# Performance work log

Hardware: AMD Instinct MI355X
Metric: run time of the kernel (lower is better)

Reference implementation:

```python
import jax, jax.numpy as jnp
import numpy as np

B, C, H, W = 16, 512, 16, 64
T = 128
V, E, EH, DH = 600, 80, 256, 512


def _lstm_scan(x_seq, h0, c0, Wih, Whh, b):
    # x_seq: [S, N, in]; PyTorch gate order i,f,g,o
    def step(carry, x):
        h, c = carry
        g = x @ Wih.T + h @ Whh.T + b
        i, f, gg, o = jnp.split(g, 4, axis=-1)
        c_new = jax.nn.sigmoid(f) * c + jax.nn.sigmoid(i) * jnp.tanh(gg)
        h_new = jax.nn.sigmoid(o) * jnp.tanh(c_new)
        return (h_new, c_new), h_new
    (hT, cT), hs = jax.lax.scan(step, (h0, c0), x_seq)
    return hs, hT, cT


def setup_inputs():
    key = jax.random.key(0)
    ks = jax.random.split(key, 32)
    INIT = 0.01
    def u(k, shape, s):
        return jax.random.uniform(k, shape, jnp.float32, -s, s)
    se = 1.0 / np.sqrt(EH)
    sd = 1.0 / np.sqrt(DH)
    sc = 1.0 / np.sqrt(DH + 2 * EH)
    so = 1.0 / np.sqrt(EH)
    sv = 1.0 / np.sqrt(2 * EH)
    return {
        'features': jax.random.normal(ks[0], (B, C, H, W), jnp.float32),
        'formulas': jax.random.randint(ks[1], (B, T), 0, V),
        'Wih_f': u(ks[2], (4 * EH, C), se), 'Whh_f': u(ks[3], (4 * EH, EH), se),
        'bih_f': u(ks[4], (4 * EH,), se), 'bhh_f': u(ks[5], (4 * EH,), se),
        'Wih_b': u(ks[6], (4 * EH, C), se), 'Whh_b': u(ks[7], (4 * EH, EH), se),
        'bih_b': u(ks[8], (4 * EH,), se), 'bhh_b': u(ks[9], (4 * EH,), se),
        'emb': jax.random.normal(ks[10], (V, E), jnp.float32),
        'Wc_w': u(ks[11], (EH, DH + 2 * EH), sc), 'Wc_b': u(ks[12], (EH,), sc),
        'Wout_w': u(ks[13], (V, EH), so), 'Wout_b': u(ks[14], (V,), so),
        'Vh0': u(ks[15], (2, EH), INIT), 'Vc0': u(ks[16], (2, EH), INIT),
        'beta': u(ks[17], (DH,), INIT),
        'Wh_w': u(ks[18], (DH, DH), sd), 'Wh_b': u(ks[19], (DH,), sd),
        'Wv_w': u(ks[20], (DH, 2 * EH), sv), 'Wv_b': u(ks[21], (DH,), sv),
        'Wdec_ih': u(ks[22], (4 * DH, EH + E), sd), 'Wdec_hh': u(ks[23], (4 * DH, DH), sd),
        'bdec_ih': u(ks[24], (4 * DH,), sd), 'bdec_hh': u(ks[25], (4 * DH,), sd),
    }


def _forward(features, formulas, Wih_f, Whh_f, bih_f, bhh_f, Wih_b, Whh_b, bih_b, bhh_b,
             emb, Wc_w, Wc_b, Wout_w, Wout_b, Vh0, Vc0, beta, Wh_w, Wh_b, Wv_w, Wv_b,
             Wdec_ih, Wdec_hh, bdec_ih, bdec_hh):
    Bv, Cv, Hv, Wd = features.shape
    eh = Vh0.shape[1]
    # ---- row encoder: bidirectional LSTM over width, batch = B*H ----
    x = features.transpose(0, 2, 3, 1).reshape(Bv * Hv, Wd, Cv).transpose(1, 0, 2)  # [W, B*H, C]
    h0f = jnp.broadcast_to(Vh0[0], (Bv * Hv, eh)); c0f = jnp.broadcast_to(Vc0[0], (Bv * Hv, eh))
    h0b = jnp.broadcast_to(Vh0[1], (Bv * Hv, eh)); c0b = jnp.broadcast_to(Vc0[1], (Bv * Hv, eh))
    hs_f, hTf, cTf = _lstm_scan(x, h0f, c0f, Wih_f, Whh_f, bih_f + bhh_f)
    hs_b, hTb, cTb = _lstm_scan(x[::-1], h0b, c0b, Wih_b, Whh_b, bih_b + bhh_b)
    hs_b = hs_b[::-1]
    enc_out = jnp.concatenate([hs_f, hs_b], -1).transpose(1, 0, 2).reshape(Bv, Hv, Wd, 2 * eh)

    def convert(s):  # [2, B*H, eh] -> [B, 2*eh]: permute, merge directions, mean over H
        return s.reshape(2, Bv, Hv, eh).transpose(1, 2, 0, 3).reshape(Bv, Hv, 2 * eh).mean(axis=1)
    h0 = convert(jnp.stack([hTf, hTb]))
    c0 = convert(jnp.stack([cTf, cTb]))
    ctx0 = enc_out.mean(axis=(1, 2))
    O0 = jnp.tanh(jnp.concatenate([h0, ctx0], 1) @ Wc_w.T + Wc_b)

    Wv_enc = enc_out @ Wv_w.T + Wv_b  # hoisted: W_v(enc_out) is constant across decode steps

    def dec_step(carry, tgt):
        h, c, O = carry
        prev_y = emb[tgt]                                   # [B, E]
        inp = jnp.concatenate([prev_y, O], 1)
        g = inp @ Wdec_ih.T + h @ Wdec_hh.T + bdec_ih + bdec_hh
        i, f, gg, o = jnp.split(g, 4, axis=-1)
        c_t = jax.nn.sigmoid(f) * c + jax.nn.sigmoid(i) * jnp.tanh(gg)
        h_t = jax.nn.sigmoid(o) * jnp.tanh(c_t)
        lin_h = h @ Wh_w.T + Wh_b                           # NB: attention uses PREVIOUS h, as in source
        e = jnp.sum(beta * jnp.tanh(lin_h[:, None, None, :] + Wv_enc), -1)  # [B, H, W]
        alpha = jax.nn.softmax(e.reshape(Bv, -1), -1).reshape(Bv, Hv, Wd)
        context = jnp.einsum('bhw,bhwd->bd', alpha, enc_out)
        O_t = jnp.tanh(jnp.concatenate([h_t, context], 1) @ Wc_w.T + Wc_b)
        logit = jax.nn.softmax(O_t @ Wout_w.T + Wout_b, -1)  # eval-mode softmax
        return (h_t, c_t, O_t), logit

    _, logits = jax.lax.scan(dec_step, (h0, c0, O0), formulas.T)
    return logits.transpose(1, 0, 2)  # [B, T, V]


def reference(features, formulas, Wih_f, Whh_f, bih_f, bhh_f, Wih_b, Whh_b, bih_b, bhh_b,
              emb, Wc_w, Wc_b, Wout_w, Wout_b, Vh0, Vc0, beta, Wh_w, Wh_b, Wv_w, Wv_b,
              Wdec_ih, Wdec_hh, bdec_ih, bdec_hh):
    logits = _forward(features, formulas, Wih_f, Whh_f, bih_f, bhh_f, Wih_b, Whh_b, bih_b, bhh_b,
                      emb, Wc_w, Wc_b, Wout_w, Wout_b, Vh0, Vc0, beta, Wh_w, Wh_b, Wv_w, Wv_b,
                      Wdec_ih, Wdec_hh, bdec_ih, bdec_hh)
    targets = jnp.argmax(logits, axis=2)  # argmax(log(p)) == argmax(p)
    return logits, targets
```

## Files before the change

### kernel.cpp

```cpp
#include <hip/hip_runtime.h>
#include <math.h>

#define NB 16
#define NC 512
#define NH 16
#define NW 64
#define NT 128
#define NV 600
#define NE 80
#define EH 256
#define DH 512
#define NSEQ 256
#define GEH 1024
#define GDH 2048

#define OFF_XPRE_F 0ull
#define OFF_XPRE_B 16777216ull
#define OFF_XT     33554432ull
#define OFF_ENC    41943040ull
#define OFF_WENC   50331648ull
#define OFF_WDT    50855936ull
#define OFF_WHT    52592640ull
#define OFF_WCT    52854784ull
#define OFF_WOUTT  53116928ull
#define OFF_HA     53270528ull
#define OFF_CENC   53532672ull
#define OFF_CDEC   53663744ull
#define OFF_CTX0   53671936ull
#define OFF_OKT    53680128ull
#define WS_FLOATS  53708800ull

__device__ __forceinline__ float sigf(float x) {
  return __builtin_amdgcn_rcpf(1.f + __expf(-x));
}
__device__ __forceinline__ float tanhfast(float x) {
  float e = __expf(2.f * x);
  return 1.f - 2.f * __builtin_amdgcn_rcpf(e + 1.f);
}

__global__ void k_transpose(float* __restrict__ dst, const float* __restrict__ src,
                            int R, int Cc) {
  int idx = blockIdx.x * 256 + threadIdx.x;
  if (idx >= R * Cc) return;
  int c = idx / R, r = idx - c * R;
  dst[idx] = src[(size_t)r * Cc + c];
}

__global__ void k_prep_wenc(float* __restrict__ dst, const float* __restrict__ whh, int dir) {
  int idx = blockIdx.x * 256 + threadIdx.x;
  int g = idx & 3, j = (idx >> 2) & 255, k = idx >> 10;
  dst[(size_t)dir * 262144 + idx] = whh[((size_t)(g * 256 + j)) * 256 + k];
}

__global__ void k_buildXt(float* __restrict__ Xt, const float* __restrict__ feat) {
  __shared__ float tile[64][65];
  int n = blockIdx.x, cb = blockIdx.y * 64;
  int b = n >> 4, hh = n & 15;
  int tid = threadIdx.x;
  for (int i = 0; i < 16; ++i) {
    int c = (tid >> 6) + i * 4;
    int w = tid & 63;
    tile[c][w] = feat[(((size_t)b * NC + cb + c) * NH + hh) * NW + w];
  }
  __syncthreads();
  for (int i = 0; i < 16; ++i) {
    int w = (tid >> 6) + i * 4;
    int ci = tid & 63;
    Xt[((size_t)(w * NSEQ + n)) * NC + cb + ci] = tile[ci][w];
  }
}

__global__ __launch_bounds__(256) void k_gemm_nt(
    const float* __restrict__ A, const float* __restrict__ Wt,
    const float* __restrict__ bias1, const float* __restrict__ bias2,
    float* __restrict__ Cout, int M, int Nn, int K) {
  __shared__ float As[128 * 32];
  __shared__ float Bs[128 * 32];
  int tid = threadIdx.x;
  int mb = blockIdx.x * 128, nb = blockIdx.y * 128;
  int tx = tid & 15, ty = tid >> 4;
  int row0 = ty * 8, col0 = tx * 8;
  float acc[8][8];
#pragma unroll
  for (int i = 0; i < 8; ++i)
#pragma unroll
    for (int j = 0; j < 8; ++j) acc[i][j] = 0.f;
  int lm = tid >> 1, lk = (tid & 1) * 8;
  int sw = 4 * ((lm >> 3) & 7);
  int p0 = (lk + sw) & 31, p1 = (lk + 4 + sw) & 31;
  const float* Ap = A + (size_t)(mb + lm) * K + lk;
  const float* Bp = Wt + (size_t)(nb + lm) * K + lk;
  for (int k0 = 0; k0 < K; k0 += 16) {
    float4 a0 = *(const float4*)(Ap + k0);
    float4 a1 = *(const float4*)(Ap + k0 + 4);
    float4 b0 = *(const float4*)(Bp + k0);
    float4 b1 = *(const float4*)(Bp + k0 + 4);
    __syncthreads();
    *(float4*)&As[lm * 32 + p0] = a0;
    *(float4*)&As[lm * 32 + p1] = a1;
    *(float4*)&Bs[lm * 32 + p0] = b0;
    *(float4*)&Bs[lm * 32 + p1] = b1;
    __syncthreads();
#pragma unroll
    for (int kq = 0; kq < 4; ++kq) {
      float4 av[8], bv[8];
#pragma unroll
      for (int i = 0; i < 8; ++i) {
        int m = row0 + i;
        av[i] = *(float4*)&As[m * 32 + ((kq * 4 + 4 * ((m >> 3) & 7)) & 31)];
      }
#pragma unroll
      for (int j = 0; j < 8; ++j) {
        int n = col0 + j;
        bv[j] = *(float4*)&Bs[n * 32 + ((kq * 4 + 4 * ((n >> 3) & 7)) & 31)];
      }
#pragma unroll
      for (int i = 0; i < 8; ++i)
#pragma unroll
        for (int j = 0; j < 8; ++j)
          acc[i][j] += av[i].x * bv[j].x + av[i].y * bv[j].y
                     + av[i].z * bv[j].z + av[i].w * bv[j].w;
    }
  }
  float bs[8];
#pragma unroll
  for (int j = 0; j < 8; ++j) {
    float v = bias1 ? bias1[nb + col0 + j] : 0.f;
    if (bias2) v += bias2[nb + col0 + j];
    bs[j] = v;
  }
  for (int i = 0; i < 8; ++i) {
    float* cp = Cout + (size_t)(mb + row0 + i) * Nn + nb + col0;
#pragma unroll
    for (int j = 0; j < 8; ++j) cp[j] = acc[i][j] + bs[j];
  }
}

__global__ __launch_bounds__(256) void k_encoder_s(
    const float* __restrict__ wenc, const float* __restrict__ xpreF,
    const float* __restrict__ xpreB, const float* __restrict__ Vh0,
    const float* __restrict__ Vc0, float* __restrict__ encout,
    float* __restrict__ hT_out, float* __restrict__ cT_out) {
  __shared__ float hs[4][256];
  int bid = blockIdx.x;
  int dir = bid >> 6;
  int s0 = (bid & 63) * 4;
  int j = threadIdx.x;
  float c[4];
  {
    float h0 = Vh0[dir * 256 + j];
    float c0v = Vc0[dir * 256 + j];
#pragma unroll
    for (int s = 0; s < 4; ++s) { hs[s][j] = h0; c[s] = c0v; }
  }
  __syncthreads();
  const float* wp = wenc + (size_t)dir * 262144 + (size_t)j * 4;
  const float* xbase = dir ? xpreB : xpreF;
  for (int t = 0; t < 64; ++t) {
    int w = dir ? (63 - t) : t;
    float acc[4][4];
#pragma unroll
    for (int s = 0; s < 4; ++s)
#pragma unroll
      for (int g = 0; g < 4; ++g) acc[s][g] = 0.f;
#pragma unroll 4
    for (int k = 0; k < 256; ++k) {
      float4 w4 = *(const float4*)(wp + (size_t)k * 1024);
      float h0k = hs[0][k], h1k = hs[1][k], h2k = hs[2][k], h3k = hs[3][k];
      acc[0][0] += w4.x * h0k; acc[0][1] += w4.y * h0k; acc[0][2] += w4.z * h0k; acc[0][3] += w4.w * h0k;
      acc[1][0] += w4.x * h1k; acc[1][1] += w4.y * h1k; acc[1][2] += w4.z * h1k; acc[1][3] += w4.w * h1k;
      acc[2][0] += w4.x * h2k; acc[2][1] += w4.y * h2k; acc[2][2] += w4.z * h2k; acc[2][3] += w4.w * h2k;
      acc[3][0] += w4.x * h3k; acc[3][1] += w4.y * h3k; acc[3][2] += w4.z * h3k; acc[3][3] += w4.w * h3k;
    }
    __syncthreads();
#pragma unroll
    for (int s = 0; s < 4; ++s) {
      int n = s0 + s;
      const float* xp = xbase + ((size_t)w * NSEQ + n) * GEH;
      float gi_ = acc[s][0] + xp[j];
      float gf_ = acc[s][1] + xp[j + 256];
      float gg_ = acc[s][2] + xp[j + 512];
      float go_ = acc[s][3] + xp[j + 768];
      float cn = sigf(gf_) * c[s] + sigf(gi_) * tanhfast(gg_);
      c[s] = cn;
      float hn = sigf(go_) * tanhfast(cn);
      hs[s][j] = hn;
      encout[((size_t)n * NW + w) * (2 * EH) + dir * EH + j] = hn;
    }
    __syncthreads();
  }
#pragma unroll
  for (int s = 0; s < 4; ++s) {
    int n = s0 + s;
    hT_out[((size_t)(dir * NSEQ + n)) * EH + j] = hs[s][j];
    cT_out[((size_t)(dir * NSEQ + n)) * EH + j] = c[s];
  }
}

__global__ void k_conv(const float* __restrict__ hA, const float* __restrict__ cE,
                       const float* __restrict__ enc, float* __restrict__ cdec,
                       float* __restrict__ okT, float* __restrict__ ctx0) {
  int b = blockIdx.x, tid = threadIdx.x;
  for (int d = tid; d < 512; d += 256) {
    float s = 0.f;
    for (int p = 0; p < 1024; ++p) s += enc[((size_t)b * 1024 + p) * 512 + d];
    ctx0[(size_t)b * 512 + d] = s * (1.f / 1024.f);
    int dir = d >> 8, u = d & 255;
    float sh = 0.f, sc_ = 0.f;
    for (int hh = 0; hh < 16; ++hh) {
      size_t idx = ((size_t)(dir * NSEQ + b * 16 + hh)) * EH + u;
      sh += hA[idx]; sc_ += cE[idx];
    }
    cdec[(size_t)b * 512 + d] = sc_ * (1.f / 16.f);
    okT[(size_t)(256 + d) * 16 + b] = sh * (1.f / 16.f);
  }
}

__global__ void k_O0v2(const float* __restrict__ okT, const float* __restrict__ ctx0,
                       const float* __restrict__ wcT, const float* __restrict__ wcb,
                       const float* __restrict__ whT, const float* __restrict__ whb,
                       float* __restrict__ okT_o, float* __restrict__ linh) {
  int b = blockIdx.x, tid = threadIdx.x;
  float a = wcb[tid];
  for (int k = 0; k < 512; ++k)
    a += okT[(size_t)(256 + k) * 16 + b] * wcT[(size_t)k * 256 + tid];
  const float* cb = ctx0 + (size_t)b * 512;
  for (int k = 0; k < 512; ++k)
    a += cb[k] * wcT[(size_t)(512 + k) * 256 + tid];
  okT_o[(size_t)tid * 16 + b] = tanhfast(a);
  for (int d = tid; d < 512; d += 256) {
    float v = whb[d];
    for (int k = 0; k < 512; ++k)
      v += okT[(size_t)(256 + k) * 16 + b] * whT[(size_t)k * 512 + d];
    linh[(size_t)b * 512 + d] = v;
  }
}

__global__ void k_embproj(const int* __restrict__ formulas, const float* __restrict__ emb,
                          const float* __restrict__ wdT, const float* __restrict__ b1,
                          const float* __restrict__ b2, float* __restrict__ ep) {
  int g = blockIdx.x * 256 + threadIdx.x;
  int tb = blockIdx.y;
  int b = tb & 15, t = tb >> 4;
  int tok = formulas[b * NT + t];
  const float* ev = emb + (size_t)tok * NE;
  float a = b1[g] + b2[g];
  for (int k = 0; k < NE; ++k) a += ev[k] * wdT[(size_t)k * GDH + g];
  ep[(size_t)tb * GDH + g] = a;
}

__device__ __forceinline__ void logits_block(
    int vc, int lane, int wq, const float* __restrict__ okT,
    const float* __restrict__ woutT, const float* __restrict__ woutb,
    float* __restrict__ ev, float* __restrict__ evp) {
  int v = vc * 64 + lane;
  bool valid = v < NV;
  int vl = valid ? v : (NV - 1);
  float acc[4] = {0.f, 0.f, 0.f, 0.f};
  for (int k = 0; k < 256; ++k) {
    float w = woutT[(size_t)k * NV + vl];
    float4 o4 = *(const float4*)&okT[(size_t)k * 16 + wq * 4];
    acc[0] += w * o4.x; acc[1] += w * o4.y; acc[2] += w * o4.z; acc[3] += w * o4.w;
  }
  float bs = woutb[vl];
#pragma unroll
  for (int i = 0; i < 4; ++i) {
    float e = valid ? __expf(acc[i] + bs) : 0.f;
    if (valid) ev[(size_t)(wq * 4 + i) * NV + v] = e;
    float s = e;
#pragma unroll
    for (int m = 1; m < 64; m <<= 1) s += __shfl_xor(s, m, 64);
    if (lane == 0) evp[(wq * 4 + i) * 16 + vc] = s;
  }
}

__device__ __forceinline__ void norm_block(
    int b, int tid, const float* __restrict__ ev, const float* __restrict__ evp,
    float* __restrict__ outp, int t) {
  float tot = 0.f;
#pragma unroll
  for (int i = 0; i < 10; ++i) tot += evp[b * 16 + i];
  float r = __builtin_amdgcn_rcpf(tot);
  float* orow = outp + ((size_t)b * NT + t) * NV;
  orow[tid] = ev[b * NV + tid] * r;
  orow[tid + 256] = ev[b * NV + tid + 256] * r;
  if (tid < 88) orow[tid + 512] = ev[b * NV + tid + 512] * r;
}

__global__ __launch_bounds__(256) void k_dec1(
    const float* __restrict__ okT, const float* __restrict__ wdT,
    const float* __restrict__ woutT, const float* __restrict__ woutb,
    const float* __restrict__ linh, const float* __restrict__ beta,
    const float* __restrict__ wvenc, const float* __restrict__ enc,
    float* __restrict__ gpart, float* __restrict__ ctxp,
    float* __restrict__ spart, float* __restrict__ ev, float* __restrict__ evp,
    int t) {
  __shared__ float smem[32];
  int bid = blockIdx.x, tid = threadIdx.x;
  int lane = tid & 63, wq = tid >> 6;

  if (bid < 512) {
    int b = bid >> 5, pc2 = bid & 31;
    int d0 = lane * 8;
    float lh[8], bt[8];
    const float* lp = linh + (size_t)b * 512 + d0;
#pragma unroll
    for (int jj = 0; jj < 8; ++jj) { lh[jj] = lp[jj]; bt[jj] = beta[d0 + jj]; }
#pragma unroll
    for (int pi = 0; pi < 8; ++pi) {
      int p = pc2 * 32 + wq * 8 + pi;
      const float* wvp = wvenc + ((size_t)(b * 1024 + p)) * 512 + d0;
      float e = 0.f;
#pragma unroll
      for (int jj = 0; jj < 8; ++jj) e += bt[jj] * tanhfast(lh[jj] + wvp[jj]);
#pragma unroll
      for (int m = 1; m < 64; m <<= 1) e += __shfl_xor(e, m, 64);
      if (lane == 0) smem[wq * 8 + pi] = __expf(e);
    }
    __syncthreads();
    float a0 = 0.f, a1 = 0.f;
    const float* erb = enc + ((size_t)(b * 1024 + pc2 * 32)) * 512 + tid * 2;
#pragma unroll 4
    for (int p = 0; p < 32; ++p) {
      float s = smem[p];
      float2 e2 = *(const float2*)(erb + (size_t)p * 512);
      a0 += s * e2.x;
      a1 += s * e2.y;
    }
    *(float2*)&ctxp[((size_t)(b * 32 + pc2)) * 512 + tid * 2] = make_float2(a0, a1);
    if (tid == 0) {
      float s = 0.f;
#pragma unroll
      for (int p = 0; p < 32; ++p) s += smem[p];
      spart[b * 32 + pc2] = s;
    }
  } else if (bid < 560) {
    int idx = bid - 512;
    int oc = idx / 6, kc = idx - oc * 6;
    int o = oc * 256 + tid, k0 = kc * 128;
    const float* wp = wdT + (size_t)(80 + k0) * GDH + o;
    const float* sp = okT + (size_t)k0 * 16;
    float acc[16];
#pragma unroll
    for (int i = 0; i < 16; ++i) acc[i] = 0.f;
    for (int kk = 0; kk < 128; ++kk) {
      float w = wp[(size_t)kk * GDH];
#pragma unroll
      for (int bb = 0; bb < 16; ++bb) acc[bb] += sp[kk * 16 + bb] * w;
    }
#pragma unroll
    for (int bb = 0; bb < 16; ++bb)
      gpart[((size_t)(kc * 16 + bb)) * GDH + o] = acc[bb];
  } else {
    if (t > 0) logits_block(bid - 560, lane, wq, okT, woutT, woutb, ev, evp);
  }
}

__global__ __launch_bounds__(256) void k_dec2(
    const float* __restrict__ gpart, const float* __restrict__ ep,
    const float* __restrict__ ctxp, const float* __restrict__ spart,
    const float* __restrict__ wcT, const float* __restrict__ wcb,
    const float* __restrict__ whT, const float* __restrict__ whb,
    const float* __restrict__ ev, const float* __restrict__ evp,
    float* __restrict__ cdecA, float* __restrict__ cdecB,
    float* __restrict__ okT, float* __restrict__ linh,
    float* __restrict__ outp, int t) {
  __shared__ float smem[1280];
  int bid = blockIdx.x, tid = threadIdx.x;
  if (bid < 64) {
    int b = bid >> 2, q = bid & 3;
    const float* cold = (t & 1) ? cdecB : cdecA;
    float* cnew = (t & 1) ? cdecA : cdecB;
    float Ssum = 0.f;
#pragma unroll
    for (int pc = 0; pc < 32; ++pc) Ssum += spart[b * 32 + pc];
    float rS = __builtin_amdgcn_rcpf(Ssum);
    {
      int d = tid * 2;
      float s0 = 0.f, s1 = 0.f;
#pragma unroll 4
      for (int pc = 0; pc < 32; ++pc) {
        float2 c2 = *(const float2*)&ctxp[((size_t)(b * 32 + pc)) * 512 + d];
        s0 += c2.x; s1 += c2.y;
      }
      smem[512 + d] = s0 * rS;
      smem[512 + d + 1] = s1 * rS;
    }
#pragma unroll
    for (int half = 0; half < 2; ++half) {
      int j = half * 256 + tid;
      float g4[4];
#pragma unroll
      for (int gi = 0; gi < 4; ++gi) {
        float v = ep[((size_t)(t * 16 + b)) * GDH + gi * 512 + j];
#pragma unroll
        for (int kc = 0; kc < 6; ++kc)
          v += gpart[((size_t)(kc * 16 + b)) * GDH + gi * 512 + j];
        g4[gi] = v;
      }
      size_t ci = (size_t)b * 512 + j;
      float cn = sigf(g4[1]) * cold[ci] + sigf(g4[0]) * tanhfast(g4[2]);
      cnew[ci] = cn;
      float hn = sigf(g4[3]) * tanhfast(cn);
      smem[j] = hn;
      okT[(size_t)(256 + j) * 16 + b] = hn;
    }
    __syncthreads();
    {
      int ol = tid & 63, kq = tid >> 6;
      int o = q * 64 + ol;
      float a = 0.f;
      const float* wp = wcT + (size_t)(kq * 256) * 256 + o;
      const float* sp = smem + kq * 256;
      for (int k = 0; k < 256; ++k) a += wp[(size_t)k * 256] * sp[k];
      smem[1024 + kq * 64 + ol] = a;
    }
    __syncthreads();
    if (tid < 64) {
      float s = smem[1024 + tid] + smem[1088 + tid] + smem[1152 + tid] + smem[1216 + tid];
      int o = q * 64 + tid;
      okT[(size_t)o * 16 + b] = tanhfast(s + wcb[o]);
    }
    __syncthreads();
    {
      int o2 = tid & 127, kh = tid >> 7;
      int o = q * 128 + o2;
      float a = 0.f;
      const float* wp = whT + (size_t)(kh * 256) * 512 + o;
      const float* sp = smem + kh * 256;
      for (int k = 0; k < 256; ++k) a += wp[(size_t)k * 512] * sp[k];
      smem[1024 + kh * 128 + o2] = a;
    }
    __syncthreads();
    if (tid < 128) {
      int o = q * 128 + tid;
      float s = smem[1024 + tid] + smem[1152 + tid];
      linh[(size_t)b * 512 + o] = s + whb[o];
    }
  } else {
    if (t > 0) norm_block(bid - 64, tid, ev, evp, outp, t - 1);
  }
}

__global__ __launch_bounds__(256) void k_log_tail(
    const float* __restrict__ okT, const float* __restrict__ woutT,
    const float* __restrict__ woutb, float* __restrict__ ev, float* __restrict__ evp) {
  int lane = threadIdx.x & 63, wq = threadIdx.x >> 6;
  logits_block(blockIdx.x, lane, wq, okT, woutT, woutb, ev, evp);
}

__global__ void k_norm(const float* __restrict__ ev, const float* __restrict__ evp,
                       float* __restrict__ outp, int t) {
  norm_block(blockIdx.x, threadIdx.x, ev, evp, outp, t);
}

__global__ void k_argmax(const float* __restrict__ outp, float* __restrict__ tgt) {
  int bt = blockIdx.x;
  int lane = threadIdx.x;
  const float* row = outp + (size_t)bt * NV;
  float bv = -1.f;
  int bi = 0;
  for (int v = lane; v < NV; v += 64) {
    float x = row[v];
    if (x > bv) { bv = x; bi = v; }
  }
#pragma unroll
  for (int m = 1; m < 64; m <<= 1) {
    float ov = __shfl_xor(bv, m, 64);
    int oi = __shfl_xor(bi, m, 64);
    if (ov > bv || (ov == bv && oi < bi)) { bv = ov; bi = oi; }
  }
  if (lane == 0) tgt[bt] = (float)bi;
}

extern "C" void kernel_launch(void* const* d_in, const int* in_sizes, int n_in,
                              void* d_out, int out_size, void* d_ws, size_t ws_size,
                              hipStream_t stream) {
  (void)in_sizes; (void)n_in; (void)out_size;
  if (ws_size < WS_FLOATS * sizeof(float)) return;

  const float* feat     = (const float*)d_in[0];
  const int*   formulas = (const int*)d_in[1];
  const float* Wih_f    = (const float*)d_in[2];
  const float* Whh_f    = (const float*)d_in[3];
  const float* bih_f    = (const float*)d_in[4];
  const float* bhh_f    = (const float*)d_in[5];
  const float* Wih_b    = (const float*)d_in[6];
  const float* Whh_b    = (const float*)d_in[7];
  const float* bih_b    = (const float*)d_in[8];
  const float* bhh_b    = (const float*)d_in[9];
  const float* emb      = (const float*)d_in[10];
  const float* Wc_w     = (const float*)d_in[11];
  const float* Wc_b     = (const float*)d_in[12];
  const float* Wout_w   = (const float*)d_in[13];
  const float* Wout_b   = (const float*)d_in[14];
  const float* Vh0      = (const float*)d_in[15];
  const float* Vc0      = (const float*)d_in[16];
  const float* beta     = (const float*)d_in[17];
  const float* Wh_w     = (const float*)d_in[18];
  const float* Wh_b     = (const float*)d_in[19];
  const float* Wv_w     = (const float*)d_in[20];
  const float* Wv_b     = (const float*)d_in[21];
  const float* Wdec_ih  = (const float*)d_in[22];
  const float* Wdec_hh  = (const float*)d_in[23];
  const float* bdec_ih  = (const float*)d_in[24];
  const float* bdec_hh  = (const float*)d_in[25];

  float* ws = (float*)d_ws;
  float* xpreF  = ws + OFF_XPRE_F;
  float* xpreB  = ws + OFF_XPRE_B;
  float* xt     = ws + OFF_XT;
  float* encout = ws + OFF_ENC;
  float* wenc   = ws + OFF_WENC;
  float* wdT    = ws + OFF_WDT;
  float* whT    = ws + OFF_WHT;
  float* wcT    = ws + OFF_WCT;
  float* woutT  = ws + OFF_WOUTT;
  float* hA     = ws + OFF_HA;
  float* cenc   = ws + OFF_CENC;
  float* cdecA  = ws + OFF_CDEC;
  float* ctx0   = ws + OFF_CTX0;
  float* okT    = ws + OFF_OKT;
  float* gpart  = xpreB;
  float* ctxp   = gpart + 196608;
  float* spart  = ctxp + 262144;
  float* ev     = spart + 512;
  float* evp    = ev + 9600;
  float* linh   = evp + 256;
  float* cdecB  = linh + 8192;
  float* embproj = xpreF;
  float* wvenc   = xt;

  float* out_logits = (float*)d_out;
  float* out_tgt    = out_logits + (size_t)NB * NT * NV;

  k_transpose<<<(2048 * 336 + 255) / 256, 256, 0, stream>>>(wdT, Wdec_ih, 2048, 336);
  k_transpose<<<(2048 * 512 + 255) / 256, 256, 0, stream>>>(wdT + 336 * 2048, Wdec_hh, 2048, 512);
  k_transpose<<<(512 * 512 + 255) / 256, 256, 0, stream>>>(whT, Wh_w, 512, 512);
  k_transpose<<<(256 * 1024 + 255) / 256, 256, 0, stream>>>(wcT, Wc_w, 256, 1024);
  k_transpose<<<(600 * 256 + 255) / 256, 256, 0, stream>>>(woutT, Wout_w, 600, 256);
  k_prep_wenc<<<1024, 256, 0, stream>>>(wenc, Whh_f, 0);
  k_prep_wenc<<<1024, 256, 0, stream>>>(wenc, Whh_b, 1);
  k_buildXt<<<dim3(256, 8), 256, 0, stream>>>(xt, feat);
  k_gemm_nt<<<dim3(128, 8), 256, 0, stream>>>(xt, Wih_f, bih_f, bhh_f, xpreF, 16384, 1024, 512);
  k_gemm_nt<<<dim3(128, 8), 256, 0, stream>>>(xt, Wih_b, bih_b, bhh_b, xpreB, 16384, 1024, 512);

  k_encoder_s<<<128, 256, 0, stream>>>(wenc, xpreF, xpreB, Vh0, Vc0, encout, hA, cenc);

  k_gemm_nt<<<dim3(128, 4), 256, 0, stream>>>(encout, Wv_w, Wv_b, nullptr, wvenc, 16384, 512, 512);
  k_conv<<<16, 256, 0, stream>>>(hA, cenc, encout, cdecA, okT, ctx0);
  k_O0v2<<<16, 256, 0, stream>>>(okT, ctx0, wcT, Wc_b, whT, Wh_b, okT, linh);
  k_embproj<<<dim3(8, 2048), 256, 0, stream>>>(formulas, emb, wdT, bdec_ih, bdec_hh, embproj);

  for (int t = 0; t < NT; ++t) {
    k_dec1<<<570, 256, 0, stream>>>(okT, wdT, woutT, Wout_b, linh, beta, wvenc, encout,
                                    gpart, ctxp, spart, ev, evp, t);
    k_dec2<<<80, 256, 0, stream>>>(gpart, embproj, ctxp, spart, wcT, Wc_b, whT, Wh_b,
                                   ev, evp, cdecA, cdecB, okT, linh, out_logits, t);
  }
  k_log_tail<<<10, 256, 0, stream>>>(okT, woutT, Wout_b, ev, evp);
  k_norm<<<16, 256, 0, stream>>>(ev, evp, out_logits, NT - 1);
  k_argmax<<<NB * NT, 64, 0, stream>>>(out_logits, out_tgt);
}
```

Measured before the change: 8.165 ms.

## Fuse decoder step kernels into one launch with intra-kernel flag synchronization

```diff
diff --git a/kernel.cpp b/kernel.cpp
--- a/kernel.cpp
+++ b/kernel.cpp
@@ -36,6 +36,18 @@
 __device__ __forceinline__ float tanhfast(float x) {
   float e = __expf(2.f * x);
   return 1.f - 2.f * __builtin_amdgcn_rcpf(e + 1.f);
+}
+
+__device__ __forceinline__ float ldc(const float* p) {
+  return __hip_atomic_load(p, __ATOMIC_RELAXED, __HIP_MEMORY_SCOPE_AGENT);
+}
+__device__ __forceinline__ void stc(float* p, float v) {
+  __hip_atomic_store(p, v, __ATOMIC_RELAXED, __HIP_MEMORY_SCOPE_AGENT);
+}
+__device__ __forceinline__ float2 ldc2(const float* p) {
+  unsigned long long u = __hip_atomic_load((const unsigned long long*)p,
+                                           __ATOMIC_RELAXED, __HIP_MEMORY_SCOPE_AGENT);
+  union { unsigned long long u; float2 f; } c; c.u = u; return c.f;
 }
 
 __global__ void k_transpose(float* __restrict__ dst, const float* __restrict__ src,
@@ -249,6 +261,37 @@
   ep[(size_t)tb * GDH + g] = a;
 }
 
+__global__ void k_zero(int* __restrict__ p, int n) {
+  int idx = blockIdx.x * 256 + threadIdx.x;
+  for (int i = idx; i < n; i += gridDim.x * 256) p[i] = 0;
+}
+
+__device__ __forceinline__ void logits_block_coh(
+    int vc, int lane, int wq, const float* __restrict__ okT,
+    const float* __restrict__ woutT, const float* __restrict__ woutb,
+    float* __restrict__ ev, float* __restrict__ evp) {
+  int v = vc * 64 + lane;
+  bool valid = v < NV;
+  int vl = valid ? v : (NV - 1);
+  float acc[4] = {0.f, 0.f, 0.f, 0.f};
+  for (int k = 0; k < 256; ++k) {
+    float w = woutT[(size_t)k * NV + vl];
+    float2 o01 = ldc2(&okT[(size_t)k * 16 + wq * 4]);
+    float2 o23 = ldc2(&okT[(size_t)k * 16 + wq * 4 + 2]);
+    acc[0] += w * o01.x; acc[1] += w * o01.y; acc[2] += w * o23.x; acc[3] += w * o23.y;
+  }
+  float bs = woutb[vl];
+#pragma unroll
+  for (int i = 0; i < 4; ++i) {
+    float e = valid ? __expf(acc[i] + bs) : 0.f;
+    if (valid) ev[(size_t)(wq * 4 + i) * NV + v] = e;
+    float s = e;
+#pragma unroll
+    for (int m = 1; m < 64; m <<= 1) s += __shfl_xor(s, m, 64);
+    if (lane == 0) evp[(wq * 4 + i) * 16 + vc] = s;
+  }
+}
+
 __device__ __forceinline__ void logits_block(
     int vc, int lane, int wq, const float* __restrict__ okT,
     const float* __restrict__ woutT, const float* __restrict__ woutb,
@@ -287,25 +330,165 @@
   if (tid < 88) orow[tid + 512] = ev[b * NV + tid + 512] * r;
 }
 
-__global__ __launch_bounds__(256) void k_dec1(
-    const float* __restrict__ okT, const float* __restrict__ wdT,
-    const float* __restrict__ woutT, const float* __restrict__ woutb,
-    const float* __restrict__ linh, const float* __restrict__ beta,
+__global__ __launch_bounds__(256, 3) void k_step(
+    float* __restrict__ okT, float* __restrict__ linh,
+    float* __restrict__ cdecA, float* __restrict__ cdecB,
+    const float* __restrict__ wdT, const float* __restrict__ whT,
+    const float* __restrict__ wcT, const float* __restrict__ woutT,
+    const float* __restrict__ whb, const float* __restrict__ beta,
+    const float* __restrict__ wcb, const float* __restrict__ woutb,
     const float* __restrict__ wvenc, const float* __restrict__ enc,
-    float* __restrict__ gpart, float* __restrict__ ctxp,
-    float* __restrict__ spart, float* __restrict__ ev, float* __restrict__ evp,
-    int t) {
-  __shared__ float smem[32];
+    const float* __restrict__ ep,
+    const float* __restrict__ gpart_r, const float* __restrict__ ctxp_r,
+    const float* __restrict__ spart_r,
+    float* __restrict__ gpart_w, float* __restrict__ ctxp_w,
+    float* __restrict__ spart_w,
+    float* __restrict__ ev_w, float* __restrict__ evp_w,
+    const float* __restrict__ ev_r, const float* __restrict__ evp_r,
+    float* __restrict__ outp, int* __restrict__ flg, int t) {
+  __shared__ float smem[1280];
   int bid = blockIdx.x, tid = threadIdx.x;
   int lane = tid & 63, wq = tid >> 6;
 
-  if (bid < 512) {
-    int b = bid >> 5, pc2 = bid & 31;
+  if (bid < 64) {
+    if (t == 0) return;
+    int tt = t - 1;
+    int b = bid >> 2, q = bid & 3;
+    const float* cold = (tt & 1) ? cdecB : cdecA;
+    float* cnew = (tt & 1) ? cdecA : cdecB;
+    float Ssum = 0.f;
+#pragma unroll
+    for (int pc = 0; pc < 32; ++pc) Ssum += spart_r[b * 32 + pc];
+    float rS = __builtin_amdgcn_rcpf(Ssum);
+    {
+      int d = tid * 2;
+      float s0 = 0.f, s1 = 0.f;
+#pragma unroll 4
+      for (int pc = 0; pc < 32; ++pc) {
+        float2 c2 = *(const float2*)&ctxp_r[((size_t)(b * 32 + pc)) * 512 + d];
+        s0 += c2.x; s1 += c2.y;
+      }
+      smem[512 + d] = s0 * rS;
+      smem[512 + d + 1] = s1 * rS;
+    }
+#pragma unroll
+    for (int half = 0; half < 2; ++half) {
+      int j = half * 256 + tid;
+      float g4[4];
+#pragma unroll
+      for (int gi = 0; gi < 4; ++gi) {
+        float v = ep[((size_t)(tt * 16 + b)) * GDH + gi * 512 + j];
+#pragma unroll
+        for (int kc = 0; kc < 6; ++kc)
+          v += gpart_r[((size_t)(kc * 16 + b)) * GDH + gi * 512 + j];
+        g4[gi] = v;
+      }
+      size_t ci = (size_t)b * 512 + j;
+      float cn = sigf(g4[1]) * cold[ci] + sigf(g4[0]) * tanhfast(g4[2]);
+      cnew[ci] = cn;
+      float hn = sigf(g4[3]) * tanhfast(cn);
+      smem[j] = hn;
+      stc(&okT[(size_t)(256 + j) * 16 + b], hn);
+    }
+    __syncthreads();
+    {
+      int ol = tid & 63, kq = tid >> 6;
+      int o = q * 64 + ol;
+      float a = 0.f;
+      const float* wp = wcT + (size_t)(kq * 256) * 256 + o;
+      const float* sp = smem + kq * 256;
+      for (int k = 0; k < 256; ++k) a += wp[(size_t)k * 256] * sp[k];
+      smem[1024 + kq * 64 + ol] = a;
+    }
+    __syncthreads();
+    if (tid < 64) {
+      float s = smem[1024 + tid] + smem[1088 + tid] + smem[1152 + tid] + smem[1216 + tid];
+      int o = q * 64 + tid;
+      stc(&okT[(size_t)o * 16 + b], tanhfast(s + wcb[o]));
+    }
+    __syncthreads();
+    {
+      int o2 = tid & 127, kh = tid >> 7;
+      int o = q * 128 + o2;
+      float a = 0.f;
+      const float* wp = whT + (size_t)(kh * 256) * 512 + o;
+      const float* sp = smem + kh * 256;
+      for (int k = 0; k < 256; ++k) a += wp[(size_t)k * 512] * sp[k];
+      smem[1024 + kh * 128 + o2] = a;
+    }
+    __syncthreads();
+    if (tid < 128) {
+      int o = q * 128 + tid;
+      float s = smem[1024 + tid] + smem[1152 + tid];
+      stc(&linh[(size_t)b * 512 + o], s + whb[o]);
+    }
+    __syncthreads();
+    if (tid == 0) {
+      __hip_atomic_fetch_add(flg + b * 32, 1, __ATOMIC_RELAXED, __HIP_MEMORY_SCOPE_AGENT);
+      __hip_atomic_fetch_add(flg + 512, 1, __ATOMIC_RELAXED, __HIP_MEMORY_SCOPE_AGENT);
+    }
+  } else if (bid < 80) {
+    if (t >= 2) norm_block(bid - 64, tid, ev_r, evp_r, outp, t - 2);
+  } else if (bid < 128) {
+    if (t > 0) {
+      if (tid == 0) {
+        int* p = flg + 512;
+        while (__hip_atomic_load(p, __ATOMIC_RELAXED, __HIP_MEMORY_SCOPE_AGENT) < 64)
+          __builtin_amdgcn_s_sleep(8);
+      }
+      __syncthreads();
+    }
+    int idx = bid - 80;
+    int oc = idx / 6, kc = idx - oc * 6;
+    int o = oc * 256 + tid, k0 = kc * 128;
+    const float* wp = wdT + (size_t)(80 + k0) * GDH + o;
+    const float* sp = okT + (size_t)k0 * 16;
+    float acc[16];
+#pragma unroll
+    for (int i = 0; i < 16; ++i) acc[i] = 0.f;
+    for (int kk = 0; kk < 128; ++kk) {
+      float w = wp[(size_t)kk * GDH];
+#pragma unroll
+      for (int h = 0; h < 8; ++h) {
+        float2 s2 = ldc2(sp + kk * 16 + h * 2);
+        acc[h * 2] += s2.x * w;
+        acc[h * 2 + 1] += s2.y * w;
+      }
+    }
+#pragma unroll
+    for (int bb = 0; bb < 16; ++bb)
+      gpart_w[((size_t)(kc * 16 + bb)) * GDH + o] = acc[bb];
+  } else if (bid < 138) {
+    if (t > 0) {
+      if (tid == 0) {
+        int* p = flg + 512;
+        while (__hip_atomic_load(p, __ATOMIC_RELAXED, __HIP_MEMORY_SCOPE_AGENT) < 64)
+          __builtin_amdgcn_s_sleep(8);
+      }
+      __syncthreads();
+      logits_block_coh(bid - 128, lane, wq, okT, woutT, woutb, ev_w, evp_w);
+    }
+  } else {
+    int idx = bid - 138;
+    int b = idx >> 5, pc2 = idx & 31;
+    if (t > 0) {
+      if (tid == 0) {
+        int* p = flg + b * 32;
+        while (__hip_atomic_load(p, __ATOMIC_RELAXED, __HIP_MEMORY_SCOPE_AGENT) < 4)
+          __builtin_amdgcn_s_sleep(8);
+      }
+      __syncthreads();
+    }
     int d0 = lane * 8;
     float lh[8], bt[8];
     const float* lp = linh + (size_t)b * 512 + d0;
 #pragma unroll
-    for (int jj = 0; jj < 8; ++jj) { lh[jj] = lp[jj]; bt[jj] = beta[d0 + jj]; }
+    for (int h = 0; h < 4; ++h) {
+      float2 l2 = ldc2(lp + h * 2);
+      lh[h * 2] = l2.x; lh[h * 2 + 1] = l2.y;
+    }
+#pragma unroll
+    for (int jj = 0; jj < 8; ++jj) bt[jj] = beta[d0 + jj];
 #pragma unroll
     for (int pi = 0; pi < 8; ++pi) {
       int p = pc2 * 32 + wq * 8 + pi;
@@ -327,32 +510,13 @@
       a0 += s * e2.x;
       a1 += s * e2.y;
     }
-    *(float2*)&ctxp[((size_t)(b * 32 + pc2)) * 512 + tid * 2] = make_float2(a0, a1);
+    *(float2*)&ctxp_w[((size_t)(b * 32 + pc2)) * 512 + tid * 2] = make_float2(a0, a1);
     if (tid == 0) {
       float s = 0.f;
 #pragma unroll
       for (int p = 0; p < 32; ++p) s += smem[p];
-      spart[b * 32 + pc2] = s;
-    }
-  } else if (bid < 560) {
-    int idx = bid - 512;
-    int oc = idx / 6, kc = idx - oc * 6;
-    int o = oc * 256 + tid, k0 = kc * 128;
-    const float* wp = wdT + (size_t)(80 + k0) * GDH + o;
-    const float* sp = okT + (size_t)k0 * 16;
-    float acc[16];
-#pragma unroll
-    for (int i = 0; i < 16; ++i) acc[i] = 0.f;
-    for (int kk = 0; kk < 128; ++kk) {
-      float w = wp[(size_t)kk * GDH];
-#pragma unroll
-      for (int bb = 0; bb < 16; ++bb) acc[bb] += sp[kk * 16 + bb] * w;
-    }
-#pragma unroll
-    for (int bb = 0; bb < 16; ++bb)
-      gpart[((size_t)(kc * 16 + bb)) * GDH + o] = acc[bb];
-  } else {
-    if (t > 0) logits_block(bid - 560, lane, wq, okT, woutT, woutb, ev, evp);
+      spart_w[b * 32 + pc2] = s;
+    }
   }
 }
 
@@ -521,13 +685,14 @@
   float* cdecA  = ws + OFF_CDEC;
   float* ctx0   = ws + OFF_CTX0;
   float* okT    = ws + OFF_OKT;
-  float* gpart  = xpreB;
-  float* ctxp   = gpart + 196608;
-  float* spart  = ctxp + 262144;
-  float* ev     = spart + 512;
-  float* evp    = ev + 9600;
-  float* linh   = evp + 256;
+  float* gp[2];  gp[0] = xpreB;            gp[1] = gp[0] + 196608;
+  float* cx[2];  cx[0] = gp[1] + 196608;   cx[1] = cx[0] + 262144;
+  float* sp2[2]; sp2[0] = cx[1] + 262144;  sp2[1] = sp2[0] + 512;
+  float* evb[2]; evb[0] = sp2[1] + 512;    evb[1] = evb[0] + 9600;
+  float* evpb[2]; evpb[0] = evb[1] + 9600; evpb[1] = evpb[0] + 256;
+  float* linh   = evpb[1] + 256;
   float* cdecB  = linh + 8192;
+  int*   dctr   = (int*)(cdecB + 8192);
   float* embproj = xpreF;
   float* wvenc   = xt;
 
@@ -551,14 +716,21 @@
   k_conv<<<16, 256, 0, stream>>>(hA, cenc, encout, cdecA, okT, ctx0);
   k_O0v2<<<16, 256, 0, stream>>>(okT, ctx0, wcT, Wc_b, whT, Wh_b, okT, linh);
   k_embproj<<<dim3(8, 2048), 256, 0, stream>>>(formulas, emb, wdT, bdec_ih, bdec_hh, embproj);
+  k_zero<<<64, 256, 0, stream>>>(dctr, 128 * 1024);
 
   for (int t = 0; t < NT; ++t) {
-    k_dec1<<<570, 256, 0, stream>>>(okT, wdT, woutT, Wout_b, linh, beta, wvenc, encout,
-                                    gpart, ctxp, spart, ev, evp, t);
-    k_dec2<<<80, 256, 0, stream>>>(gpart, embproj, ctxp, spart, wcT, Wc_b, whT, Wh_b,
-                                   ev, evp, cdecA, cdecB, okT, linh, out_logits, t);
-  }
-  k_log_tail<<<10, 256, 0, stream>>>(okT, woutT, Wout_b, ev, evp);
-  k_norm<<<16, 256, 0, stream>>>(ev, evp, out_logits, NT - 1);
+    int w = t & 1, r = (t - 1) & 1;
+    k_step<<<650, 256, 0, stream>>>(okT, linh, cdecA, cdecB,
+                                    wdT, whT, wcT, woutT, Wh_b, beta, Wc_b, Wout_b,
+                                    wvenc, encout, embproj,
+                                    gp[r], cx[r], sp2[r],
+                                    gp[w], cx[w], sp2[w],
+                                    evb[w], evpb[w], evb[r], evpb[r],
+                                    out_logits, dctr + t * 1024, t);
+  }
+  k_dec2<<<80, 256, 0, stream>>>(gp[1], embproj, cx[1], sp2[1], wcT, Wc_b, whT, Wh_b,
+                                 evb[1], evpb[1], cdecA, cdecB, okT, linh, out_logits, 127);
+  k_log_tail<<<10, 256, 0, stream>>>(okT, woutT, Wout_b, evb[0], evpb[0]);
+  k_norm<<<16, 256, 0, stream>>>(evb[0], evpb[0], out_logits, NT - 1);
   k_argmax<<<NB * NT, 64, 0, stream>>>(out_logits, out_tgt);
 }
```

Result: slower. 9.468 ms (+16.0%).

## Split encoder recurrence K-loop across 4 thread groups and widen dec1 attention blocks

Applied to the files above, without the earlier changes.

```diff
diff --git a/kernel.cpp b/kernel.cpp
--- a/kernel.cpp
+++ b/kernel.cpp
@@ -136,25 +136,27 @@
   }
 }
 
-__global__ __launch_bounds__(256) void k_encoder_s(
+__global__ __launch_bounds__(1024) void k_encoder_s(
     const float* __restrict__ wenc, const float* __restrict__ xpreF,
     const float* __restrict__ xpreB, const float* __restrict__ Vh0,
     const float* __restrict__ Vc0, float* __restrict__ encout,
     float* __restrict__ hT_out, float* __restrict__ cT_out) {
   __shared__ float hs[4][256];
+  __shared__ float pacc[3][16][256];
   int bid = blockIdx.x;
   int dir = bid >> 6;
   int s0 = (bid & 63) * 4;
-  int j = threadIdx.x;
+  int tid = threadIdx.x;
+  int j = tid & 255, kq = tid >> 8;
   float c[4];
-  {
+  if (kq == 0) {
     float h0 = Vh0[dir * 256 + j];
     float c0v = Vc0[dir * 256 + j];
 #pragma unroll
     for (int s = 0; s < 4; ++s) { hs[s][j] = h0; c[s] = c0v; }
   }
   __syncthreads();
-  const float* wp = wenc + (size_t)dir * 262144 + (size_t)j * 4;
+  const float* wp = wenc + (size_t)dir * 262144 + (size_t)(kq * 64) * 1024 + (size_t)j * 4;
   const float* xbase = dir ? xpreB : xpreF;
   for (int t = 0; t < 64; ++t) {
     int w = dir ? (63 - t) : t;
@@ -163,37 +165,50 @@
     for (int s = 0; s < 4; ++s)
 #pragma unroll
       for (int g = 0; g < 4; ++g) acc[s][g] = 0.f;
-#pragma unroll 4
-    for (int k = 0; k < 256; ++k) {
+#pragma unroll 8
+    for (int k = 0; k < 64; ++k) {
       float4 w4 = *(const float4*)(wp + (size_t)k * 1024);
-      float h0k = hs[0][k], h1k = hs[1][k], h2k = hs[2][k], h3k = hs[3][k];
+      int kk = kq * 64 + k;
+      float h0k = hs[0][kk], h1k = hs[1][kk], h2k = hs[2][kk], h3k = hs[3][kk];
       acc[0][0] += w4.x * h0k; acc[0][1] += w4.y * h0k; acc[0][2] += w4.z * h0k; acc[0][3] += w4.w * h0k;
       acc[1][0] += w4.x * h1k; acc[1][1] += w4.y * h1k; acc[1][2] += w4.z * h1k; acc[1][3] += w4.w * h1k;
       acc[2][0] += w4.x * h2k; acc[2][1] += w4.y * h2k; acc[2][2] += w4.z * h2k; acc[2][3] += w4.w * h2k;
       acc[3][0] += w4.x * h3k; acc[3][1] += w4.y * h3k; acc[3][2] += w4.z * h3k; acc[3][3] += w4.w * h3k;
     }
-    __syncthreads();
+    if (kq > 0) {
+#pragma unroll
+      for (int s = 0; s < 4; ++s)
+#pragma unroll
+        for (int g = 0; g < 4; ++g)
+          pacc[kq - 1][s * 4 + g][j] = acc[s][g];
+    }
+    __syncthreads();
+    if (kq == 0) {
+#pragma unroll
+      for (int s = 0; s < 4; ++s) {
+        int n = s0 + s;
+        const float* xp = xbase + ((size_t)w * NSEQ + n) * GEH;
+        float g4[4];
+#pragma unroll
+        for (int g = 0; g < 4; ++g)
+          g4[g] = acc[s][g] + pacc[0][s * 4 + g][j] + pacc[1][s * 4 + g][j]
+                + pacc[2][s * 4 + g][j] + xp[g * 256 + j];
+        float cn = sigf(g4[1]) * c[s] + sigf(g4[0]) * tanhfast(g4[2]);
+        c[s] = cn;
+        float hn = sigf(g4[3]) * tanhfast(cn);
+        hs[s][j] = hn;
+        encout[((size_t)n * NW + w) * (2 * EH) + dir * EH + j] = hn;
+      }
+    }
+    __syncthreads();
+  }
+  if (kq == 0) {
 #pragma unroll
     for (int s = 0; s < 4; ++s) {
       int n = s0 + s;
-      const float* xp = xbase + ((size_t)w * NSEQ + n) * GEH;
-      float gi_ = acc[s][0] + xp[j];
-      float gf_ = acc[s][1] + xp[j + 256];
-      float gg_ = acc[s][2] + xp[j + 512];
-      float go_ = acc[s][3] + xp[j + 768];
-      float cn = sigf(gf_) * c[s] + sigf(gi_) * tanhfast(gg_);
-      c[s] = cn;
-      float hn = sigf(go_) * tanhfast(cn);
-      hs[s][j] = hn;
-      encout[((size_t)n * NW + w) * (2 * EH) + dir * EH + j] = hn;
-    }
-    __syncthreads();
-  }
-#pragma unroll
-  for (int s = 0; s < 4; ++s) {
-    int n = s0 + s;
-    hT_out[((size_t)(dir * NSEQ + n)) * EH + j] = hs[s][j];
-    cT_out[((size_t)(dir * NSEQ + n)) * EH + j] = c[s];
+      hT_out[((size_t)(dir * NSEQ + n)) * EH + j] = hs[s][j];
+      cT_out[((size_t)(dir * NSEQ + n)) * EH + j] = c[s];
+    }
   }
 }
 
@@ -287,7 +302,7 @@
   if (tid < 88) orow[tid + 512] = ev[b * NV + tid + 512] * r;
 }
 
-__global__ __launch_bounds__(256) void k_dec1(
+__global__ __launch_bounds__(512) void k_dec1(
     const float* __restrict__ okT, const float* __restrict__ wdT,
     const float* __restrict__ woutT, const float* __restrict__ woutb,
     const float* __restrict__ linh, const float* __restrict__ beta,
@@ -295,7 +310,8 @@
     float* __restrict__ gpart, float* __restrict__ ctxp,
     float* __restrict__ spart, float* __restrict__ ev, float* __restrict__ evp,
     int t) {
-  __shared__ float smem[32];
+  __shared__ float sscore[32];
+  __shared__ float cpart[2][512];
   int bid = blockIdx.x, tid = threadIdx.x;
   int lane = tid & 63, wq = tid >> 6;
 
@@ -307,52 +323,64 @@
 #pragma unroll
     for (int jj = 0; jj < 8; ++jj) { lh[jj] = lp[jj]; bt[jj] = beta[d0 + jj]; }
 #pragma unroll
-    for (int pi = 0; pi < 8; ++pi) {
-      int p = pc2 * 32 + wq * 8 + pi;
+    for (int pi = 0; pi < 4; ++pi) {
+      int p = pc2 * 32 + wq * 4 + pi;
       const float* wvp = wvenc + ((size_t)(b * 1024 + p)) * 512 + d0;
       float e = 0.f;
 #pragma unroll
       for (int jj = 0; jj < 8; ++jj) e += bt[jj] * tanhfast(lh[jj] + wvp[jj]);
 #pragma unroll
       for (int m = 1; m < 64; m <<= 1) e += __shfl_xor(e, m, 64);
-      if (lane == 0) smem[wq * 8 + pi] = __expf(e);
-    }
-    __syncthreads();
+      if (lane == 0) sscore[wq * 4 + pi] = __expf(e);
+    }
+    __syncthreads();
+    int hh = tid >> 8;
+    int dd = (tid & 255) * 2;
     float a0 = 0.f, a1 = 0.f;
-    const float* erb = enc + ((size_t)(b * 1024 + pc2 * 32)) * 512 + tid * 2;
+    const float* erb = enc + ((size_t)(b * 1024 + pc2 * 32 + hh * 16)) * 512 + dd;
 #pragma unroll 4
-    for (int p = 0; p < 32; ++p) {
-      float s = smem[p];
+    for (int p = 0; p < 16; ++p) {
+      float s = sscore[hh * 16 + p];
       float2 e2 = *(const float2*)(erb + (size_t)p * 512);
       a0 += s * e2.x;
       a1 += s * e2.y;
     }
-    *(float2*)&ctxp[((size_t)(b * 32 + pc2)) * 512 + tid * 2] = make_float2(a0, a1);
-    if (tid == 0) {
-      float s = 0.f;
-#pragma unroll
-      for (int p = 0; p < 32; ++p) s += smem[p];
-      spart[b * 32 + pc2] = s;
+    cpart[hh][dd] = a0;
+    cpart[hh][dd + 1] = a1;
+    __syncthreads();
+    if (tid < 256) {
+      int d = tid * 2;
+      *(float2*)&ctxp[((size_t)(b * 32 + pc2)) * 512 + d] =
+          make_float2(cpart[0][d] + cpart[1][d], cpart[0][d + 1] + cpart[1][d + 1]);
+      if (tid == 0) {
+        float s = 0.f;
+#pragma unroll
+        for (int p = 0; p < 32; ++p) s += sscore[p];
+        spart[b * 32 + pc2] = s;
+      }
     }
   } else if (bid < 560) {
-    int idx = bid - 512;
-    int oc = idx / 6, kc = idx - oc * 6;
-    int o = oc * 256 + tid, k0 = kc * 128;
-    const float* wp = wdT + (size_t)(80 + k0) * GDH + o;
-    const float* sp = okT + (size_t)k0 * 16;
-    float acc[16];
-#pragma unroll
-    for (int i = 0; i < 16; ++i) acc[i] = 0.f;
-    for (int kk = 0; kk < 128; ++kk) {
-      float w = wp[(size_t)kk * GDH];
-#pragma unroll
-      for (int bb = 0; bb < 16; ++bb) acc[bb] += sp[kk * 16 + bb] * w;
-    }
-#pragma unroll
-    for (int bb = 0; bb < 16; ++bb)
-      gpart[((size_t)(kc * 16 + bb)) * GDH + o] = acc[bb];
+    if (tid < 256) {
+      int idx = bid - 512;
+      int oc = idx / 6, kc = idx - oc * 6;
+      int o = oc * 256 + tid, k0 = kc * 128;
+      const float* wp = wdT + (size_t)(80 + k0) * GDH + o;
+      const float* sp = okT + (size_t)k0 * 16;
+      float acc[16];
+#pragma unroll
+      for (int i = 0; i < 16; ++i) acc[i] = 0.f;
+      for (int kk = 0; kk < 128; ++kk) {
+        float w = wp[(size_t)kk * GDH];
+#pragma unroll
+        for (int bb = 0; bb < 16; ++bb) acc[bb] += sp[kk * 16 + bb] * w;
+      }
+#pragma unroll
+      for (int bb = 0; bb < 16; ++bb)
+        gpart[((size_t)(kc * 16 + bb)) * GDH + o] = acc[bb];
+    }
   } else {
-    if (t > 0) logits_block(bid - 560, lane, wq, okT, woutT, woutb, ev, evp);
+    if (tid < 256 && t > 0)
+      logits_block(bid - 560, lane, wq, okT, woutT, woutb, ev, evp);
   }
 }
 
@@ -545,7 +573,7 @@
   k_gemm_nt<<<dim3(128, 8), 256, 0, stream>>>(xt, Wih_f, bih_f, bhh_f, xpreF, 16384, 1024, 512);
   k_gemm_nt<<<dim3(128, 8), 256, 0, stream>>>(xt, Wih_b, bih_b, bhh_b, xpreB, 16384, 1024, 512);
 
-  k_encoder_s<<<128, 256, 0, stream>>>(wenc, xpreF, xpreB, Vh0, Vc0, encout, hA, cenc);
+  k_encoder_s<<<128, 1024, 0, stream>>>(wenc, xpreF, xpreB, Vh0, Vc0, encout, hA, cenc);
 
   k_gemm_nt<<<dim3(128, 4), 256, 0, stream>>>(encout, Wv_w, Wv_b, nullptr, wvenc, 16384, 512, 512);
   k_conv<<<16, 256, 0, stream>>>(hA, cenc, encout, cdecA, okT, ctx0);
@@ -553,7 +581,7 @@
   k_embproj<<<dim3(8, 2048), 256, 0, stream>>>(formulas, emb, wdT, bdec_ih, bdec_hh, embproj);
 
   for (int t = 0; t < NT; ++t) {
-    k_dec1<<<570, 256, 0, stream>>>(okT, wdT, woutT, Wout_b, linh, beta, wvenc, encout,
+    k_dec1<<<570, 512, 0, stream>>>(okT, wdT, woutT, Wout_b, linh, beta, wvenc, encout,
                                     gpart, ctxp, spart, ev, evp, t);
     k_dec2<<<80, 256, 0, stream>>>(gpart, embproj, ctxp, spart, wcT, Wc_b, whT, Wh_b,
                                    ev, evp, cdecA, cdecB, okT, linh, out_logits, t);
```

Result: no change. 8.277 ms (+1.4%).
